# Kernel tuning notes

Hardware: AMD Instinct MI355X
Metric: run time of the kernel (lower is better)

The kernel has to match this reference:

```python
import jax, jax.numpy as jnp
import numpy as np

B, S, D = 1, 4096, 1024
H, DH = 8, 128
SCALING = 256.0 ** -0.5
SOFTCAP = 50.0
WINDOW = 512
EPS = 1e-6
NEG = -1e30


def setup_inputs() -> dict:
    key = jax.random.key(0)
    ks = jax.random.split(key, 8)
    hidden_states = jax.random.normal(ks[0], (B, S, D), dtype=jnp.float32)
    # rope tables: plausible cos/sin in [-1,1]
    inv_freq = 1.0 / (10000.0 ** (jnp.arange(0, DH, 2, dtype=jnp.float32) / DH))
    t = jnp.arange(S, dtype=jnp.float32)
    freqs = jnp.outer(t, inv_freq)  # [S, DH/2]
    emb = jnp.concatenate([freqs, freqs], axis=-1)  # [S, DH]
    cos = jnp.cos(emb)[None]  # [1, S, DH]
    sin = jnp.sin(emb)[None]
    w = 0.02
    Wq = jax.random.normal(ks[1], (H * DH, D), dtype=jnp.float32) * w
    Wk = jax.random.normal(ks[2], (H * DH, D), dtype=jnp.float32) * w
    Wv = jax.random.normal(ks[3], (H * DH, D), dtype=jnp.float32) * w
    Wo = jax.random.normal(ks[4], (D, H * DH), dtype=jnp.float32) * w
    q_norm_w = jnp.zeros((DH,), dtype=jnp.float32)
    k_norm_w = jnp.zeros((DH,), dtype=jnp.float32)
    return {"hidden_states": hidden_states, "cos": cos, "sin": sin,
            "Wq": Wq, "Wk": Wk, "Wv": Wv, "Wo": Wo,
            "q_norm_w": q_norm_w, "k_norm_w": k_norm_w}


def _rms_norm(x, w):
    # Gemma3 RMSNorm: x * rsqrt(mean(x^2) + eps) * (1 + w)
    var = jnp.mean(jnp.square(x), axis=-1, keepdims=True)
    return x * jax.lax.rsqrt(var + EPS) * (1.0 + w)


def _rotate_half(x):
    x1, x2 = jnp.split(x, 2, axis=-1)
    return jnp.concatenate([-x2, x1], axis=-1)


def reference(hidden_states, cos, sin, Wq, Wk, Wv, Wo, q_norm_w, k_norm_w):
    b, s, _ = hidden_states.shape
    # QKV projections -> [B, H, S, DH]
    q = (hidden_states @ Wq.T).reshape(b, s, H, DH).transpose(0, 2, 1, 3)
    k = (hidden_states @ Wk.T).reshape(b, s, H, DH).transpose(0, 2, 1, 3)
    v = (hidden_states @ Wv.T).reshape(b, s, H, DH).transpose(0, 2, 1, 3)
    # per-head RMSNorm on q and k
    q = _rms_norm(q, q_norm_w)
    k = _rms_norm(k, k_norm_w)
    # RoPE (cos/sin broadcast over heads via unsqueeze(1))
    c = cos[:, None, :, :]
    si = sin[:, None, :, :]
    q = q * c + _rotate_half(q) * si
    k = k * c + _rotate_half(k) * si
    # scores with scaling and logit softcapping
    scores = jnp.einsum('bhqd,bhkd->bhqk', q, k) * SCALING
    scores = SOFTCAP * jnp.tanh(scores / SOFTCAP)
    # causal + sliding-window mask: attend to j with 0 <= i - j < WINDOW (plus j == i)
    i = jnp.arange(s)[:, None]
    j = jnp.arange(s)[None, :]
    mask = (j <= i) & (i - j < WINDOW)  # [S, S]
    scores = jnp.where(mask[None, None], scores, NEG)
    probs = jax.nn.softmax(scores, axis=-1)  # [B, H, S, S]
    attn = jnp.einsum('bhqk,bhkd->bhqd', probs, v)
    attn = attn.transpose(0, 2, 1, 3).reshape(b, s, H * DH)
    out = attn @ Wo.T
    return out, probs
```

## Files before the change

kernel.cpp:

```cpp
#include <hip/hip_runtime.h>

#define S_LEN 4096

typedef _Float16 f16;
typedef __bf16 bf16;
typedef __attribute__((ext_vector_type(4))) _Float16 f16x4;
typedef __attribute__((ext_vector_type(8))) _Float16 f16x8;
typedef __attribute__((ext_vector_type(8))) __bf16 bf16x8;
typedef __attribute__((ext_vector_type(4))) float f32x4;

__device__ __forceinline__ void async_cp16(void* lds, const void* g) {
  __builtin_amdgcn_global_load_lds((const __attribute__((address_space(1))) void*)g,
                                   (__attribute__((address_space(3))) void*)lds, 16, 0, 0);
}

__device__ __forceinline__ f32x4 mfma16(f16x8 a, f16x8 b, f32x4 c) {
  return __builtin_amdgcn_mfma_f32_16x16x32_f16(a, b, c, 0, 0, 0);
}

__global__ void detect_dtype(const unsigned short* __restrict__ x, int* __restrict__ flag) {
  const int t = threadIdx.x;
  int cnt = 0;
  for (int i = t; i < 16384; i += 256) {
    const int e = (x[i] >> 7) & 0xFF;
    cnt += (e >= 0x87);
  }
#pragma unroll
  for (int m = 1; m < 64; m <<= 1) cnt += __shfl_xor(cnt, m);
  __shared__ int red[4];
  if ((t & 63) == 0) red[t >> 6] = cnt;
  __syncthreads();
  if (t == 0) *flag = (red[0] + red[1] + red[2] + red[3] > 64) ? 1 : 0;
}

__device__ __forceinline__ void cvt8(const void* src, f16* dst, int i, int fp) {
  f16x8 o;
  if (fp) {
    const float* s = (const float*)src;
#pragma unroll
    for (int j = 0; j < 8; ++j) o[j] = (f16)s[i + j];
  } else {
    const bf16x8 v = *(const bf16x8*)((const bf16*)src + i);
#pragma unroll
    for (int j = 0; j < 8; ++j) o[j] = (f16)(float)v[j];
  }
  *(f16x8*)(dst + i) = o;
}

__global__ void cvt_all(const void* __restrict__ hs, const void* __restrict__ wq,
                        const void* __restrict__ wk, const void* __restrict__ wv,
                        const void* __restrict__ wo, const void* __restrict__ c,
                        const void* __restrict__ s, const void* __restrict__ qn,
                        const void* __restrict__ kn, f16* __restrict__ hsf,
                        f16* __restrict__ wqkv, f16* __restrict__ woh,
                        float* __restrict__ cd, float* __restrict__ sd,
                        float* __restrict__ qnd, float* __restrict__ knd,
                        const int* __restrict__ flagp) {
  const int fp = *flagp;
  const int b = blockIdx.x, tid = threadIdx.x;
  if (b < 2048) {
    cvt8(hs, hsf, (b * 256 + tid) * 8, fp);
  } else if (b < 4096) {
    const int bb = b - 2048;
    const int sub = bb >> 9;
    const int i = ((bb & 511) * 256 + tid) * 8;
    const void* src = (sub == 0) ? wq : (sub == 1) ? wk : (sub == 2) ? wv : wo;
    f16* dst = (sub < 3) ? (wqkv + (size_t)sub * 1048576) : woh;
    cvt8(src, dst, i, fp);
  } else if (b < 8192) {
    const int bb = b - 4096;
    const void* src = (bb < 2048) ? c : s;
    float* dst = (bb < 2048) ? cd : sd;
    const int i = (bb & 2047) * 256 + tid;
    dst[i] = fp ? ((const float*)src)[i] : (float)((const bf16*)src)[i];
  } else {
    if (tid < 128) qnd[tid] = fp ? ((const float*)qn)[tid] : (float)((const bf16*)qn)[tid];
    else knd[tid - 128] = fp ? ((const float*)kn)[tid - 128] : (float)((const bf16*)kn)[tid - 128];
  }
}

template <int MODE>
__launch_bounds__(256, 1)
__global__ void gemm128(const f16* __restrict__ A, const f16* __restrict__ B,
                        void* __restrict__ Cv, int K, int N, const int* __restrict__ flagp) {
  __shared__ f16 As[128 * 64];
  __shared__ f16 Bs[128 * 64];
  const int tid = threadIdx.x;
  const int w = tid >> 6, l = tid & 63;
  const int n0 = blockIdx.x * 128, m0 = blockIdx.y * 128;
  const int wm = (w >> 1) * 64, wn = (w & 1) * 64;
  const int fp = flagp ? *flagp : 0;
  f32x4 acc[4][4] = {};
  for (int k0 = 0; k0 < K; k0 += 64) {
#pragma unroll
    for (int it = 0; it < 4; ++it) {
      const int c = it * 4 + w;
      const int row = c * 8 + (l >> 3);
      const int dq = (l & 7) ^ (row & 7);
      async_cp16(&As[c * 512], &A[(size_t)(m0 + row) * K + k0 + dq * 8]);
      async_cp16(&Bs[c * 512], &B[(size_t)(n0 + row) * K + k0 + dq * 8]);
    }
    __syncthreads();
#pragma unroll
    for (int ks = 0; ks < 2; ++ks) {
      f16x8 af[4], bfr[4];
#pragma unroll
      for (int i = 0; i < 4; ++i) {
        const int ra = wm + i * 16 + (l & 15);
        af[i] = *(const f16x8*)&As[ra * 64 + (((ks * 4 + (l >> 4)) ^ (ra & 7)) << 3)];
        const int rb = wn + i * 16 + (l & 15);
        bfr[i] = *(const f16x8*)&Bs[rb * 64 + (((ks * 4 + (l >> 4)) ^ (rb & 7)) << 3)];
      }
#pragma unroll
      for (int mi = 0; mi < 4; ++mi)
#pragma unroll
        for (int ni = 0; ni < 4; ++ni)
          acc[mi][ni] = mfma16(af[mi], bfr[ni], acc[mi][ni]);
    }
    __syncthreads();
  }
#pragma unroll
  for (int mi = 0; mi < 4; ++mi)
#pragma unroll
    for (int ni = 0; ni < 4; ++ni) {
      const int col = n0 + wn + ni * 16 + (l & 15);
      const int row = m0 + wm + mi * 16 + ((l >> 4) << 2);
#pragma unroll
      for (int r = 0; r < 4; ++r) {
        const size_t off = (size_t)(row + r) * N + col;
        if (MODE == 1)      ((f16*)Cv)[off] = (f16)acc[mi][ni][r];
        else if (fp)        ((float*)Cv)[off] = acc[mi][ni][r];
        else                ((bf16*)Cv)[off] = (bf16)acc[mi][ni][r];
      }
    }
}

__global__ void rope_rms2(const f16* __restrict__ QKV, const float* __restrict__ cosp,
                          const float* __restrict__ sinp, const float* __restrict__ qnw,
                          const float* __restrict__ knw, f16* __restrict__ qh,
                          f16* __restrict__ kh) {
  const int w = threadIdx.x >> 6, l = threadIdx.x & 63;
  const int p = blockIdx.x * 4 + w;
  const int s = p >> 3, h = p & 7;
  const int part = blockIdx.y;
  const float* nw = part ? knw : qnw;
  f16* outb = part ? kh : qh;
  const f16* xr = QKV + (size_t)s * 3072 + part * 1024 + h * 128;
  const float x0 = (float)xr[l], x1 = (float)xr[l + 64];
  float ss = x0 * x0 + x1 * x1;
#pragma unroll
  for (int m = 1; m < 64; m <<= 1) ss += __shfl_xor(ss, m);
  const float r = rsqrtf(ss * (1.f / 128.f) + 1e-6f);
  const float g0 = r * (1.f + nw[l]);
  const float g1 = r * (1.f + nw[l + 64]);
  const float c0 = cosp[s * 128 + l], c1 = cosp[s * 128 + l + 64];
  const float s0 = sinp[s * 128 + l], s1 = sinp[s * 128 + l + 64];
  const float xn0 = x0 * g0, xn1 = x1 * g1;
  f16* o = outb + ((size_t)h * S_LEN + s) * 128;
  o[l] = (f16)(xn0 * c0 - xn1 * s0);
  o[l + 64] = (f16)(xn1 * c1 + xn0 * s1);
}

__global__ void vtrans(const f16* __restrict__ vh, f16* __restrict__ vt) {
  __shared__ f16 tle[64][65];
  const int s0 = blockIdx.x * 64, n0 = blockIdx.y * 64;
  const int tid = threadIdx.x;
#pragma unroll
  for (int i = 0; i < 16; ++i) {
    const int idx = i * 256 + tid;
    tle[idx >> 6][idx & 63] = vh[(size_t)(s0 + (idx >> 6)) * 3072 + 2048 + n0 + (idx & 63)];
  }
  __syncthreads();
  const int h = n0 >> 7, dh0 = n0 & 127;
#pragma unroll
  for (int i = 0; i < 16; ++i) {
    const int idx = i * 256 + tid;
    vt[((size_t)h * 128 + dh0 + (idx >> 6)) * S_LEN + s0 + (idx & 63)] = tle[idx & 63][idx >> 6];
  }
}

__launch_bounds__(256, 2)
__global__ void attn64(const f16* __restrict__ Qh, const f16* __restrict__ Kh,
                       const f16* __restrict__ Vt, f16* __restrict__ Pc,
                       float* __restrict__ Lsg, f16* __restrict__ Oh) {
  __shared__ f16 Qs[64 * 128];
  __shared__ f16 Ks[2 * 64 * 128];
  __shared__ f16 Vs[2 * 128 * 64];
  const int tid = threadIdx.x, w = tid >> 6, l = tid & 63;
  const int q0 = blockIdx.x * 64, h = blockIdx.y;
  const int kt0 = (q0 >= 512) ? ((q0 - 511) >> 6) : 0;
  const int kt1 = (q0 + 64) >> 6;

#pragma unroll
  for (int it = 0; it < 4; ++it) {
    const int c = it * 4 + w;
    const int row = c * 4 + (l >> 4);
    const int dq = (l & 15) ^ (row & 15);
    async_cp16(&Qs[c * 512], &Qh[((size_t)h * S_LEN + q0 + row) * 128 + dq * 8]);
  }
#pragma unroll
  for (int it = 0; it < 4; ++it) {
    const int c = it * 4 + w;
    { const int row = c * 4 + (l >> 4);
      const int dq = (l & 15) ^ (row & 15);
      async_cp16(&Ks[c * 512], &Kh[((size_t)h * S_LEN + kt0 * 64 + row) * 128 + dq * 8]); }
    { const int row = c * 8 + (l >> 3);
      const int dq = (l & 7) ^ (row & 7);
      async_cp16(&Vs[c * 512], &Vt[((size_t)h * 128 + row) * S_LEN + kt0 * 64 + dq * 8]); }
  }
  __syncthreads();
  f16x8 qfrag[4];
#pragma unroll
  for (int ks = 0; ks < 4; ++ks) {
    const int r = w * 16 + (l & 15);
    qfrag[ks] = *(const f16x8*)&Qs[r * 128 + (((ks * 4 + (l >> 4)) ^ (r & 15)) << 3)];
  }
  __syncthreads();

  f16* Ps = Qs + w * 1024;
  float l_i[4] = {0.f, 0.f, 0.f, 0.f};
  f32x4 oacc[8] = {};

  for (int t = kt0; t < kt1; ++t) {
    const int cur = (t - kt0) & 1;
    const int kb = cur * 8192, vb = cur * 8192;
    if (t + 1 < kt1) {
      const int nb = (cur ^ 1) * 8192;
#pragma unroll
      for (int it = 0; it < 4; ++it) {
        const int c = it * 4 + w;
        { const int row = c * 4 + (l >> 4);
          const int dq = (l & 15) ^ (row & 15);
          async_cp16(&Ks[nb + c * 512],
                     &Kh[((size_t)h * S_LEN + (t + 1) * 64 + row) * 128 + dq * 8]); }
        { const int row = c * 8 + (l >> 3);
          const int dq = (l & 7) ^ (row & 7);
          async_cp16(&Vs[nb + c * 512],
                     &Vt[((size_t)h * 128 + row) * S_LEN + (t + 1) * 64 + dq * 8]); }
      }
    }
    f32x4 sacc[4] = {};
#pragma unroll
    for (int ks = 0; ks < 4; ++ks) {
      f16x8 kfrag[4];
#pragma unroll
      for (int ni = 0; ni < 4; ++ni) {
        const int r = ni * 16 + (l & 15);
        kfrag[ni] = *(const f16x8*)&Ks[kb + r * 128 + (((ks * 4 + (l >> 4)) ^ (r & 15)) << 3)];
      }
#pragma unroll
      for (int ni = 0; ni < 4; ++ni)
        sacc[ni] = mfma16(qfrag[ks], kfrag[ni], sacc[ni]);
    }
#pragma unroll
    for (int reg = 0; reg < 4; ++reg) {
      const int pr = ((l >> 4) << 2) + reg;
      const int q = q0 + w * 16 + pr;
      float rs = 0.f;
#pragma unroll
      for (int ni = 0; ni < 4; ++ni) {
        const int col = t * 64 + ni * 16 + (l & 15);
        float s = sacc[ni][reg] * 0.0625f;
        const float z = __expf(s * 0.04f);
        s = 50.f * (1.f - 2.f / (z + 1.f));
        const bool valid = (col <= q) && (q - col < 512);
        const float p = valid ? __expf(s - 8.f) : 0.f;
        rs += p;
        const int pc = ni * 16 + (l & 15);
        Ps[pr * 64 + (((pc >> 3) ^ (pr & 7)) << 3) + (pc & 7)] = (f16)p;
      }
#pragma unroll
      for (int m = 1; m < 16; m <<= 1) rs += __shfl_xor(rs, m);
      l_i[reg] += rs;
    }
#pragma unroll
    for (int ks = 0; ks < 2; ++ks) {
      const int rp = l & 15;
      const f16x8 pf = *(const f16x8*)&Ps[rp * 64 + (((ks * 4 + (l >> 4)) ^ (rp & 7)) << 3)];
      f16x8 vf[8];
#pragma unroll
      for (int ni = 0; ni < 8; ++ni) {
        const int r = ni * 16 + (l & 15);
        vf[ni] = *(const f16x8*)&Vs[vb + r * 64 + (((ks * 4 + (l >> 4)) ^ (r & 7)) << 3)];
      }
#pragma unroll
      for (int ni = 0; ni < 8; ++ni)
        oacc[ni] = mfma16(pf, vf[ni], oacc[ni]);
    }
    {
      const size_t rowbase = (size_t)h * 4096 + q0 + w * 16;
#pragma unroll
      for (int i = 0; i < 4; ++i) {
        const int pr = i * 4 + (l >> 4);
        const int pc = (l & 15) * 4;
        const f16x4 v = *(const f16x4*)&Ps[pr * 64 + (((pc >> 3) ^ (pr & 7)) << 3) + (pc & 7)];
        *(f16x4*)&Pc[(rowbase + pr) * 576 + (t - kt0) * 64 + pc] = v;
      }
    }
    __syncthreads();
  }

  float il[4];
#pragma unroll
  for (int r = 0; r < 4; ++r) il[r] = 1.f / l_i[r];
  if ((l & 15) == 0) {
#pragma unroll
    for (int r = 0; r < 4; ++r)
      Lsg[(h << 12) + q0 + w * 16 + ((l >> 4) << 2) + r] = il[r];
  }
#pragma unroll
  for (int ni = 0; ni < 8; ++ni) {
    const int row = q0 + w * 16 + ((l >> 4) << 2);
    const int col = h * 128 + ni * 16 + (l & 15);
#pragma unroll
    for (int r = 0; r < 4; ++r)
      Oh[(size_t)(row + r) * 1024 + col] = (f16)(oacc[ni][r] * il[r]);
  }
}

__launch_bounds__(256)
__global__ void probs_write(const f16* __restrict__ Pc, const float* __restrict__ Lsg,
                            void* __restrict__ dout, const int* __restrict__ flagp) {
  const int fp = *flagp;
  const long long stride = (long long)gridDim.x * 256;
  if (fp) {
    float* pb = (float*)dout + 4194304;
    const long long total = 8LL * 4096 * 1024;
    for (long long idx = (long long)blockIdx.x * 256 + threadIdx.x; idx < total; idx += stride) {
      const int h = (int)(idx >> 22);
      const int rem = (int)(idx & 4194303);
      const int row = rem >> 10;
      const int c = (rem & 1023) << 2;
      const int q0 = row & ~63;
      const int jc0 = (q0 >= 512) ? (((q0 - 511) >> 6) << 6) : 0;
      f32x4 v = {};
      if (c >= jc0 && c < q0 + 64) {
        const float sc = Lsg[(h << 12) + row];
        const f16x4 pv = *(const f16x4*)&Pc[((size_t)(h << 12) + row) * 576 + (c - jc0)];
#pragma unroll
        for (int k = 0; k < 4; ++k) v[k] = (float)pv[k] * sc;
      }
      *(f32x4*)&pb[((size_t)h << 24) + ((size_t)row << 12) + c] = v;
    }
  } else {
    bf16* pb = (bf16*)dout + 4194304;
    const long long total = 8LL * 4096 * 512;
    for (long long idx = (long long)blockIdx.x * 256 + threadIdx.x; idx < total; idx += stride) {
      const int h = (int)(idx >> 21);
      const int rem = (int)(idx & 2097151);
      const int row = rem >> 9;
      const int c = (rem & 511) << 3;
      const int q0 = row & ~63;
      const int jc0 = (q0 >= 512) ? (((q0 - 511) >> 6) << 6) : 0;
      bf16x8 v = {};
      if (c >= jc0 && c < q0 + 64) {
        const float sc = Lsg[(h << 12) + row];
        const f16x8 pv = *(const f16x8*)&Pc[((size_t)(h << 12) + row) * 576 + (c - jc0)];
#pragma unroll
        for (int k = 0; k < 8; ++k) v[k] = (bf16)((float)pv[k] * sc);
      }
      *(bf16x8*)&pb[((size_t)h << 24) + ((size_t)row << 12) + c] = v;
    }
  }
}

extern "C" void kernel_launch(void* const* d_in, const int* in_sizes, int n_in,
                              void* d_out, int out_size, void* d_ws, size_t ws_size,
                              hipStream_t stream) {
  (void)in_sizes; (void)n_in; (void)out_size; (void)ws_size;
  char* ws = (char*)d_ws;
  f16*   Pc    = (f16*)(ws);
  f16*   qkv   = (f16*)(ws);
  f16*   qh    = (f16*)(ws + (36u << 20));
  f16*   kh    = (f16*)(ws + (44u << 20));
  f16*   vt    = (f16*)(ws + (52u << 20));
  f16*   attnh = (f16*)(ws + (60u << 20));
  f16*   woh   = (f16*)(ws + (68u << 20));
  f16*   hsf   = (f16*)(ws + (70u << 20));
  float* Lsg   = (float*)(ws + (70u << 20));
  f16*   wqkv  = (f16*)(ws + (78u << 20));
  float* cosf  = (float*)(ws + (84u << 20));
  float* sinf  = (float*)(ws + (86u << 20));
  float* qnwf  = (float*)(ws + (88u << 20));
  float* knwf  = (float*)(ws + (88u << 20) + 512);
  int*   flag  = (int*)(ws + (88u << 20) + 1024);

  detect_dtype<<<1, 256, 0, stream>>>((const unsigned short*)d_in[0], flag);
  cvt_all<<<8193, 256, 0, stream>>>(d_in[0], d_in[3], d_in[4], d_in[5], d_in[6],
                                    d_in[1], d_in[2], d_in[7], d_in[8],
                                    hsf, wqkv, woh, cosf, sinf, qnwf, knwf, flag);

  gemm128<1><<<dim3(24, 32), 256, 0, stream>>>(hsf, wqkv, qkv, 1024, 3072, flag);
  rope_rms2<<<dim3(8192, 2), 256, 0, stream>>>(qkv, cosf, sinf, qnwf, knwf, qh, kh);
  vtrans<<<dim3(64, 16), 256, 0, stream>>>(qkv, vt);
  attn64<<<dim3(64, 8), 256, 0, stream>>>(qh, kh, vt, Pc, Lsg, attnh);
  probs_write<<<4096, 256, 0, stream>>>(Pc, Lsg, d_out, flag);
  gemm128<3><<<dim3(8, 32), 256, 0, stream>>>(attnh, woh, d_out, 1024, 1024, flag);
}
```

Baseline: 727.6 us.

## Fuse RMSNorm/RoPE/V-transpose into QKV GEMM epilogue and merge O-proj with probs write

The QKV GEMM epilogue now stages the tile in shared memory and directly applies per-head RMSNorm and RoPE for Q/K, or transposes V, removing the separate rope and transpose kernels and the f16 QKV round trip. The output projection and the large probs write are merged into one launch so the GEMM blocks overlap with the bandwidth-bound store, which now uses nontemporal stores and 2x unrolling. s_setprio hints are added around the MFMA phases in attention, and occupancy is raised to 2 blocks per CU for the GEMMs. The cost is more register and shared-memory pressure in the fused kernels.

```diff
diff --git a/kernel.cpp b/kernel.cpp
--- a/kernel.cpp
+++ b/kernel.cpp
@@ -79,26 +79,27 @@
   }
 }
 
-template <int MODE>
-__launch_bounds__(256, 1)
-__global__ void gemm128(const f16* __restrict__ A, const f16* __restrict__ B,
-                        void* __restrict__ Cv, int K, int N, const int* __restrict__ flagp) {
-  __shared__ f16 As[128 * 64];
-  __shared__ f16 Bs[128 * 64];
+__launch_bounds__(256, 2)
+__global__ void gemm_qkv(const f16* __restrict__ A, const f16* __restrict__ B,
+                         const float* __restrict__ cosp, const float* __restrict__ sinp,
+                         const float* __restrict__ qnw, const float* __restrict__ knw,
+                         f16* __restrict__ qh, f16* __restrict__ kh, f16* __restrict__ vt) {
+  __shared__ f16 smem[16384];
+  f16* As = smem;
+  f16* Bs = smem + 8192;
   const int tid = threadIdx.x;
   const int w = tid >> 6, l = tid & 63;
   const int n0 = blockIdx.x * 128, m0 = blockIdx.y * 128;
   const int wm = (w >> 1) * 64, wn = (w & 1) * 64;
-  const int fp = flagp ? *flagp : 0;
   f32x4 acc[4][4] = {};
-  for (int k0 = 0; k0 < K; k0 += 64) {
+  for (int k0 = 0; k0 < 1024; k0 += 64) {
 #pragma unroll
     for (int it = 0; it < 4; ++it) {
       const int c = it * 4 + w;
       const int row = c * 8 + (l >> 3);
       const int dq = (l & 7) ^ (row & 7);
-      async_cp16(&As[c * 512], &A[(size_t)(m0 + row) * K + k0 + dq * 8]);
-      async_cp16(&Bs[c * 512], &B[(size_t)(n0 + row) * K + k0 + dq * 8]);
+      async_cp16(&As[c * 512], &A[(size_t)(m0 + row) * 1024 + k0 + dq * 8]);
+      async_cp16(&Bs[c * 512], &B[(size_t)(n0 + row) * 1024 + k0 + dq * 8]);
     }
     __syncthreads();
 #pragma unroll
@@ -119,63 +120,54 @@
     }
     __syncthreads();
   }
+  const int part = blockIdx.x >> 3;
+  const int h = blockIdx.x & 7;
 #pragma unroll
   for (int mi = 0; mi < 4; ++mi)
 #pragma unroll
     for (int ni = 0; ni < 4; ++ni) {
-      const int col = n0 + wn + ni * 16 + (l & 15);
-      const int row = m0 + wm + mi * 16 + ((l >> 4) << 2);
+      const int col = wn + ni * 16 + (l & 15);
 #pragma unroll
       for (int r = 0; r < 4; ++r) {
-        const size_t off = (size_t)(row + r) * N + col;
-        if (MODE == 1)      ((f16*)Cv)[off] = (f16)acc[mi][ni][r];
-        else if (fp)        ((float*)Cv)[off] = acc[mi][ni][r];
-        else                ((bf16*)Cv)[off] = (bf16)acc[mi][ni][r];
-      }
-    }
-}
-
-__global__ void rope_rms2(const f16* __restrict__ QKV, const float* __restrict__ cosp,
-                          const float* __restrict__ sinp, const float* __restrict__ qnw,
-                          const float* __restrict__ knw, f16* __restrict__ qh,
-                          f16* __restrict__ kh) {
-  const int w = threadIdx.x >> 6, l = threadIdx.x & 63;
-  const int p = blockIdx.x * 4 + w;
-  const int s = p >> 3, h = p & 7;
-  const int part = blockIdx.y;
-  const float* nw = part ? knw : qnw;
-  f16* outb = part ? kh : qh;
-  const f16* xr = QKV + (size_t)s * 3072 + part * 1024 + h * 128;
-  const float x0 = (float)xr[l], x1 = (float)xr[l + 64];
-  float ss = x0 * x0 + x1 * x1;
-#pragma unroll
-  for (int m = 1; m < 64; m <<= 1) ss += __shfl_xor(ss, m);
-  const float r = rsqrtf(ss * (1.f / 128.f) + 1e-6f);
-  const float g0 = r * (1.f + nw[l]);
-  const float g1 = r * (1.f + nw[l + 64]);
-  const float c0 = cosp[s * 128 + l], c1 = cosp[s * 128 + l + 64];
-  const float s0 = sinp[s * 128 + l], s1 = sinp[s * 128 + l + 64];
-  const float xn0 = x0 * g0, xn1 = x1 * g1;
-  f16* o = outb + ((size_t)h * S_LEN + s) * 128;
-  o[l] = (f16)(xn0 * c0 - xn1 * s0);
-  o[l + 64] = (f16)(xn1 * c1 + xn0 * s1);
-}
-
-__global__ void vtrans(const f16* __restrict__ vh, f16* __restrict__ vt) {
-  __shared__ f16 tle[64][65];
-  const int s0 = blockIdx.x * 64, n0 = blockIdx.y * 64;
-  const int tid = threadIdx.x;
-#pragma unroll
-  for (int i = 0; i < 16; ++i) {
-    const int idx = i * 256 + tid;
-    tle[idx >> 6][idx & 63] = vh[(size_t)(s0 + (idx >> 6)) * 3072 + 2048 + n0 + (idx & 63)];
-  }
+        const int row = wm + mi * 16 + ((l >> 4) << 2) + r;
+        smem[row * 128 + (col ^ (((row >> 3) & 7) << 3))] = (f16)acc[mi][ni][r];
+      }
+    }
   __syncthreads();
-  const int h = n0 >> 7, dh0 = n0 & 127;
-#pragma unroll
-  for (int i = 0; i < 16; ++i) {
-    const int idx = i * 256 + tid;
-    vt[((size_t)h * 128 + dh0 + (idx >> 6)) * S_LEN + s0 + (idx & 63)] = tle[idx & 63][idx >> 6];
+  if (part == 2) {
+#pragma unroll
+    for (int it = 0; it < 8; ++it) {
+      const int idx = it * 256 + tid;
+      const int dh = idx >> 4;
+      const int sl = (idx & 15) * 8;
+      f16x8 o;
+#pragma unroll
+      for (int k = 0; k < 8; ++k)
+        o[k] = smem[(sl + k) * 128 + (dh ^ ((((sl + k) >> 3) & 7) << 3))];
+      *(f16x8*)&vt[((size_t)(h * 128 + dh)) * S_LEN + m0 + sl] = o;
+    }
+  } else {
+    const float* nw = part ? knw : qnw;
+    f16* outb = part ? kh : qh;
+    const float nw0 = 1.f + nw[l], nw1 = 1.f + nw[l + 64];
+#pragma unroll 4
+    for (int rr = 0; rr < 32; ++rr) {
+      const int row = w * 32 + rr;
+      const int sg = m0 + row;
+      const int cs = ((row >> 3) & 7) << 3;
+      const float x0 = (float)smem[row * 128 + (l ^ cs)];
+      const float x1 = (float)smem[row * 128 + ((l + 64) ^ cs)];
+      float ssum = x0 * x0 + x1 * x1;
+#pragma unroll
+      for (int m = 1; m < 64; m <<= 1) ssum += __shfl_xor(ssum, m);
+      const float rn = rsqrtf(ssum * (1.f / 128.f) + 1e-6f);
+      const float g0 = rn * nw0, g1 = rn * nw1;
+      const float c0 = cosp[sg * 128 + l], c1 = cosp[sg * 128 + l + 64];
+      const float s0 = sinp[sg * 128 + l], s1 = sinp[sg * 128 + l + 64];
+      f16* o = outb + ((size_t)h * S_LEN + sg) * 128;
+      o[l] = (f16)(x0 * g0 * c0 - x1 * g1 * s0);
+      o[l + 64] = (f16)(x1 * g1 * c1 + x0 * g0 * s1);
+    }
   }
 }
 
@@ -240,6 +232,7 @@
       }
     }
     f32x4 sacc[4] = {};
+    __builtin_amdgcn_s_setprio(1);
 #pragma unroll
     for (int ks = 0; ks < 4; ++ks) {
       f16x8 kfrag[4];
@@ -252,6 +245,7 @@
       for (int ni = 0; ni < 4; ++ni)
         sacc[ni] = mfma16(qfrag[ks], kfrag[ni], sacc[ni]);
     }
+    __builtin_amdgcn_s_setprio(0);
 #pragma unroll
     for (int reg = 0; reg < 4; ++reg) {
       const int pr = ((l >> 4) << 2) + reg;
@@ -273,6 +267,7 @@
       for (int m = 1; m < 16; m <<= 1) rs += __shfl_xor(rs, m);
       l_i[reg] += rs;
     }
+    __builtin_amdgcn_s_setprio(1);
 #pragma unroll
     for (int ks = 0; ks < 2; ++ks) {
       const int rp = l & 15;
@@ -287,6 +282,7 @@
       for (int ni = 0; ni < 8; ++ni)
         oacc[ni] = mfma16(pf, vf[ni], oacc[ni]);
     }
+    __builtin_amdgcn_s_setprio(0);
     {
       const size_t rowbase = (size_t)h * 4096 + q0 + w * 16;
 #pragma unroll
@@ -318,48 +314,110 @@
   }
 }
 
-__launch_bounds__(256)
-__global__ void probs_write(const f16* __restrict__ Pc, const float* __restrict__ Lsg,
-                            void* __restrict__ dout, const int* __restrict__ flagp) {
+__launch_bounds__(256, 2)
+__global__ void gemmO_probs(const f16* __restrict__ A, const f16* __restrict__ B,
+                            void* __restrict__ dout, const f16* __restrict__ Pc,
+                            const float* __restrict__ Lsg, const int* __restrict__ flagp) {
+  __shared__ f16 smem[16384];
   const int fp = *flagp;
-  const long long stride = (long long)gridDim.x * 256;
-  if (fp) {
-    float* pb = (float*)dout + 4194304;
-    const long long total = 8LL * 4096 * 1024;
-    for (long long idx = (long long)blockIdx.x * 256 + threadIdx.x; idx < total; idx += stride) {
-      const int h = (int)(idx >> 22);
-      const int rem = (int)(idx & 4194303);
-      const int row = rem >> 10;
-      const int c = (rem & 1023) << 2;
-      const int q0 = row & ~63;
-      const int jc0 = (q0 >= 512) ? (((q0 - 511) >> 6) << 6) : 0;
-      f32x4 v = {};
-      if (c >= jc0 && c < q0 + 64) {
-        const float sc = Lsg[(h << 12) + row];
-        const f16x4 pv = *(const f16x4*)&Pc[((size_t)(h << 12) + row) * 576 + (c - jc0)];
-#pragma unroll
-        for (int k = 0; k < 4; ++k) v[k] = (float)pv[k] * sc;
-      }
-      *(f32x4*)&pb[((size_t)h << 24) + ((size_t)row << 12) + c] = v;
-    }
+  const int tid = threadIdx.x;
+  if (blockIdx.x < 256) {
+    f16* As = smem;
+    f16* Bs = smem + 8192;
+    const int w = tid >> 6, l = tid & 63;
+    const int n0 = (blockIdx.x & 7) * 128, m0 = (blockIdx.x >> 3) * 128;
+    const int wm = (w >> 1) * 64, wn = (w & 1) * 64;
+    f32x4 acc[4][4] = {};
+    for (int k0 = 0; k0 < 1024; k0 += 64) {
+#pragma unroll
+      for (int it = 0; it < 4; ++it) {
+        const int c = it * 4 + w;
+        const int row = c * 8 + (l >> 3);
+        const int dq = (l & 7) ^ (row & 7);
+        async_cp16(&As[c * 512], &A[(size_t)(m0 + row) * 1024 + k0 + dq * 8]);
+        async_cp16(&Bs[c * 512], &B[(size_t)(n0 + row) * 1024 + k0 + dq * 8]);
+      }
+      __syncthreads();
+#pragma unroll
+      for (int ks = 0; ks < 2; ++ks) {
+        f16x8 af[4], bfr[4];
+#pragma unroll
+        for (int i = 0; i < 4; ++i) {
+          const int ra = wm + i * 16 + (l & 15);
+          af[i] = *(const f16x8*)&As[ra * 64 + (((ks * 4 + (l >> 4)) ^ (ra & 7)) << 3)];
+          const int rb = wn + i * 16 + (l & 15);
+          bfr[i] = *(const f16x8*)&Bs[rb * 64 + (((ks * 4 + (l >> 4)) ^ (rb & 7)) << 3)];
+        }
+#pragma unroll
+        for (int mi = 0; mi < 4; ++mi)
+#pragma unroll
+          for (int ni = 0; ni < 4; ++ni)
+            acc[mi][ni] = mfma16(af[mi], bfr[ni], acc[mi][ni]);
+      }
+      __syncthreads();
+    }
+#pragma unroll
+    for (int mi = 0; mi < 4; ++mi)
+#pragma unroll
+      for (int ni = 0; ni < 4; ++ni) {
+        const int col = n0 + wn + ni * 16 + (l & 15);
+        const int row = m0 + wm + mi * 16 + ((l >> 4) << 2);
+#pragma unroll
+        for (int r = 0; r < 4; ++r) {
+          const size_t off = (size_t)(row + r) * 1024 + col;
+          if (fp) ((float*)dout)[off] = acc[mi][ni][r];
+          else    ((bf16*)dout)[off] = (bf16)acc[mi][ni][r];
+        }
+      }
   } else {
-    bf16* pb = (bf16*)dout + 4194304;
-    const long long total = 8LL * 4096 * 512;
-    for (long long idx = (long long)blockIdx.x * 256 + threadIdx.x; idx < total; idx += stride) {
-      const int h = (int)(idx >> 21);
-      const int rem = (int)(idx & 2097151);
-      const int row = rem >> 9;
-      const int c = (rem & 511) << 3;
-      const int q0 = row & ~63;
-      const int jc0 = (q0 >= 512) ? (((q0 - 511) >> 6) << 6) : 0;
-      bf16x8 v = {};
-      if (c >= jc0 && c < q0 + 64) {
-        const float sc = Lsg[(h << 12) + row];
-        const f16x8 pv = *(const f16x8*)&Pc[((size_t)(h << 12) + row) * 576 + (c - jc0)];
-#pragma unroll
-        for (int k = 0; k < 8; ++k) v[k] = (bf16)((float)pv[k] * sc);
-      }
-      *(bf16x8*)&pb[((size_t)h << 24) + ((size_t)row << 12) + c] = v;
+    const long long stride = (long long)(gridDim.x - 256) * 256;
+    const long long base = (long long)(blockIdx.x - 256) * 256 + tid;
+    if (fp) {
+      float* pb = (float*)dout + 4194304;
+      const long long total = 8LL * 4096 * 1024;
+      auto do4 = [&](long long idx) {
+        const int h = (int)(idx >> 22);
+        const int rem = (int)(idx & 4194303);
+        const int row = rem >> 10;
+        const int c = (rem & 1023) << 2;
+        const int q0r = row & ~63;
+        const int jc0 = (q0r >= 512) ? (((q0r - 511) >> 6) << 6) : 0;
+        f32x4 v = {};
+        if (c >= jc0 && c < q0r + 64) {
+          const float sc = Lsg[(h << 12) + row];
+          const f16x4 pv = *(const f16x4*)&Pc[((size_t)(h << 12) + row) * 576 + (c - jc0)];
+#pragma unroll
+          for (int k = 0; k < 4; ++k) v[k] = (float)pv[k] * sc;
+        }
+        __builtin_nontemporal_store(v, (f32x4*)&pb[((size_t)h << 24) + ((size_t)row << 12) + c]);
+      };
+      for (long long i0 = base; i0 < total; i0 += 2 * stride) {
+        do4(i0);
+        if (i0 + stride < total) do4(i0 + stride);
+      }
+    } else {
+      bf16* pb = (bf16*)dout + 4194304;
+      const long long total = 8LL * 4096 * 512;
+      auto do8 = [&](long long idx) {
+        const int h = (int)(idx >> 21);
+        const int rem = (int)(idx & 2097151);
+        const int row = rem >> 9;
+        const int c = (rem & 511) << 3;
+        const int q0r = row & ~63;
+        const int jc0 = (q0r >= 512) ? (((q0r - 511) >> 6) << 6) : 0;
+        bf16x8 v = {};
+        if (c >= jc0 && c < q0r + 64) {
+          const float sc = Lsg[(h << 12) + row];
+          const f16x8 pv = *(const f16x8*)&Pc[((size_t)(h << 12) + row) * 576 + (c - jc0)];
+#pragma unroll
+          for (int k = 0; k < 8; ++k) v[k] = (bf16)((float)pv[k] * sc);
+        }
+        __builtin_nontemporal_store(v, (bf16x8*)&pb[((size_t)h << 24) + ((size_t)row << 12) + c]);
+      };
+      for (long long i0 = base; i0 < total; i0 += 2 * stride) {
+        do8(i0);
+        if (i0 + stride < total) do8(i0 + stride);
+      }
     }
   }
 }
@@ -370,7 +428,6 @@
   (void)in_sizes; (void)n_in; (void)out_size; (void)ws_size;
   char* ws = (char*)d_ws;
   f16*   Pc    = (f16*)(ws);
-  f16*   qkv   = (f16*)(ws);
   f16*   qh    = (f16*)(ws + (36u << 20));
   f16*   kh    = (f16*)(ws + (44u << 20));
   f16*   vt    = (f16*)(ws + (52u << 20));
@@ -389,11 +446,7 @@
   cvt_all<<<8193, 256, 0, stream>>>(d_in[0], d_in[3], d_in[4], d_in[5], d_in[6],
                                     d_in[1], d_in[2], d_in[7], d_in[8],
                                     hsf, wqkv, woh, cosf, sinf, qnwf, knwf, flag);
-
-  gemm128<1><<<dim3(24, 32), 256, 0, stream>>>(hsf, wqkv, qkv, 1024, 3072, flag);
-  rope_rms2<<<dim3(8192, 2), 256, 0, stream>>>(qkv, cosf, sinf, qnwf, knwf, qh, kh);
-  vtrans<<<dim3(64, 16), 256, 0, stream>>>(qkv, vt);
+  gemm_qkv<<<dim3(24, 32), 256, 0, stream>>>(hsf, wqkv, cosf, sinf, qnwf, knwf, qh, kh, vt);
   attn64<<<dim3(64, 8), 256, 0, stream>>>(qh, kh, vt, Pc, Lsg, attnh);
-  probs_write<<<4096, 256, 0, stream>>>(Pc, Lsg, d_out, flag);
-  gemm128<3><<<dim3(8, 32), 256, 0, stream>>>(attnh, woh, d_out, 1024, 1024, flag);
-}
+  gemmO_probs<<<2048, 256, 0, stream>>>(attnh, woh, d_out, Pc, Lsg, flag);
+}
```

After: 670.1 us. 7.9% less time.
